# Performance work log

Hardware: AMD Instinct MI355X
Metric: run time of the kernel (lower is better)

## Reference

```python
import jax, jax.numpy as jnp
import numpy as np

H = 2048   # hidden_size
L = 512    # latent_dim
B, S = 4, 2048

def setup_inputs() -> dict:
    key = jax.random.key(0)
    ks = jax.random.split(key, 13)
    def lin(k, fan_in, shape):
        bound = 1.0 / np.sqrt(fan_in)
        return jax.random.uniform(k, shape, jnp.float32, -bound, bound)
    return {
        "hidden_states": jax.random.normal(ks[0], (B, S, H), jnp.float32),
        "num_reasoning_steps": 8,
        # to_latent: Linear(H, 2L) -> ReLU -> Linear(2L, L)
        "W_enc1": lin(ks[1], H, (2 * L, H)), "b_enc1": lin(ks[2], H, (2 * L,)),
        "W_enc2": lin(ks[3], 2 * L, (L, 2 * L)), "b_enc2": lin(ks[4], 2 * L, (L,)),
        # from_latent: Linear(L, 2L) -> ReLU -> Linear(2L, H)
        "W_dec1": lin(ks[5], L, (2 * L, L)), "b_dec1": lin(ks[6], L, (2 * L,)),
        "W_dec2": lin(ks[7], 2 * L, (H, 2 * L)), "b_dec2": lin(ks[8], 2 * L, (H,)),
        # GRUCell(L, L): weight_ih/hh [3L, L], bias_ih/hh [3L]
        "w_ih": lin(ks[9], L, (3 * L, L)), "w_hh": lin(ks[10], L, (3 * L, L)),
        "b_ih": lin(ks[11], L, (3 * L,)), "b_hh": lin(ks[12], L, (3 * L,)),
    }

def _gru_cell(x, h, w_ih, w_hh, b_ih, b_hh):
    # PyTorch GRUCell semantics
    gi = x @ w_ih.T + b_ih   # [*, 3L]
    gh = h @ w_hh.T + b_hh
    i_r, i_z, i_n = jnp.split(gi, 3, axis=-1)
    h_r, h_z, h_n = jnp.split(gh, 3, axis=-1)
    r = jax.nn.sigmoid(i_r + h_r)
    z = jax.nn.sigmoid(i_z + h_z)
    n = jnp.tanh(i_n + r * h_n)
    return (1.0 - z) * n + z * h

def reference(hidden_states, num_reasoning_steps, W_enc1, b_enc1, W_enc2, b_enc2,
              W_dec1, b_dec1, W_dec2, b_dec2, w_ih, w_hh, b_ih, b_hh):
    # encode to latent
    latent = jax.nn.relu(hidden_states @ W_enc1.T + b_enc1) @ W_enc2.T + b_enc2  # [B,S,L]

    def step(lat, _):
        lat = _gru_cell(lat, lat, w_ih, w_hh, b_ih, b_hh)
        return lat, lat

    latent, traj = jax.lax.scan(step, latent, None, length=num_reasoning_steps)
    # traj: [steps, B, S, L] -> [B, S, steps, L]
    latent_trajectory = jnp.transpose(traj, (1, 2, 0, 3))
    decoded = jax.nn.relu(latent @ W_dec1.T + b_dec1) @ W_dec2.T + b_dec2  # [B,S,H]
    return decoded, latent_trajectory
```

## Files before the change

### kernel.cpp

```cpp
#include <hip/hip_runtime.h>
#include <hip/hip_bf16.h>
#include <cstdint>
#include <cstddef>

#define TOKENS   8192
#define HID      2048
#define LAT      512
#define LAT2     1024
#define GCOLS    2048
#define STEPS    8
#define DEC_ELEMS (TOKENS*HID)

typedef __attribute__((ext_vector_type(8))) __bf16 bf16x8;
typedef __attribute__((ext_vector_type(4))) float  f32x4;

__device__ __forceinline__ unsigned short f32_to_bf16_rne(float f) {
  unsigned int u = __float_as_uint(f);
  unsigned int r = (u + 0x7FFFu + ((u >> 16) & 1u)) >> 16;
  return (unsigned short)r;
}

__device__ __forceinline__ float sigmoidf_(float x) {
  if (x >= 0.f) { float e = __expf(-x); return 1.f / (1.f + e); }
  float e = __expf(x); return e / (1.f + e);
}
__device__ __forceinline__ float tanhf_(float x) {
  float ax = fabsf(x);
  float e  = __expf(-2.f * ax);
  float t  = (1.f - e) / (1.f + e);
  return copysignf(t, x);
}

__device__ __forceinline__ void gl_lds16(const void* g, void* l) {
  __builtin_amdgcn_global_load_lds(
      (const __attribute__((address_space(1))) void*)g,
      (__attribute__((address_space(3))) void*)l, 16, 0, 0);
}

__global__ void k_cast(const float* __restrict__ s, unsigned short* __restrict__ d, int n4) {
  int i = blockIdx.x * blockDim.x + threadIdx.x;
  int stride = gridDim.x * blockDim.x;
  for (; i < n4; i += stride) {
    float4 v = ((const float4*)s)[i];
    ushort4 o;
    o.x = f32_to_bf16_rne(v.x);
    o.y = f32_to_bf16_rne(v.y);
    o.z = f32_to_bf16_rne(v.z);
    o.w = f32_to_bf16_rne(v.w);
    ((ushort4*)d)[i] = o;
  }
}

__global__ void k_gru_pack(const float* __restrict__ wih, const float* __restrict__ whh,
                           const float* __restrict__ bih, const float* __restrict__ bhh,
                           unsigned short* __restrict__ Wg, float* __restrict__ biasg) {
  int gc = blockIdx.x;
  int l  = gc >> 2;
  int g  = gc & 3;
  int row = (g == 0) ? l : (g == 1) ? (512 + l) : (1024 + l);
  for (int c = threadIdx.x; c < LAT; c += blockDim.x) {
    float v;
    if (g <= 1)      v = wih[row * LAT + c] + whh[row * LAT + c];
    else if (g == 2) v = wih[row * LAT + c];
    else             v = whh[row * LAT + c];
    Wg[(size_t)gc * LAT + c] = f32_to_bf16_rne(v);
  }
  if (threadIdx.x == 0) {
    float b;
    if (g <= 1)      b = bih[row] + bhh[row];
    else if (g == 2) b = bih[row];
    else             b = bhh[row];
    biasg[gc] = b;
  }
}

#define MWG 128
#define NWG 128
#define KTILE 64

template <int EPI>
__global__ __launch_bounds__(256)
void gemm_bt(const unsigned short* __restrict__ A,
             const unsigned short* __restrict__ W,
             const float* __restrict__ bias,
             int K, int N,
             float* __restrict__ outF,
             unsigned short* __restrict__ outB,
             const float* __restrict__ hIn,
             float* __restrict__ traj,
             int step) {
  __shared__ __align__(16) char smem[2 * MWG * KTILE * 2];
  unsigned short* As = (unsigned short*)smem;
  unsigned short* Bs = As + MWG * KTILE;

  const int tid  = threadIdx.x;
  const int lane = tid & 63;
  const int wv   = tid >> 6;
  const int wr   = wv >> 1;
  const int wc   = wv & 1;
  const int m0   = blockIdx.x * MWG;
  const int n0   = blockIdx.y * NWG;

  const int lr = lane & 15;
  const int lq = lane >> 4;

  const int srow = lane >> 3;
  const int scol = (lane & 7) * 8;

  f32x4 acc[4][4];
#pragma unroll
  for (int i = 0; i < 4; ++i)
#pragma unroll
    for (int j = 0; j < 4; ++j) acc[i][j] = (f32x4){0.f, 0.f, 0.f, 0.f};

  const unsigned short* Ab = A + (size_t)m0 * K;
  const unsigned short* Wb = W + (size_t)n0 * K;

  const int KT = K / KTILE;
  for (int kt = 0; kt < KT; ++kt) {
    const int k0 = kt * KTILE;
#pragma unroll
    for (int q = 0; q < 4; ++q) {
      int row = 32 * wv + 8 * q + srow;
      gl_lds16(Ab + (size_t)row * K + k0 + scol, As + (32 * wv + 8 * q) * KTILE);
      gl_lds16(Wb + (size_t)row * K + k0 + scol, Bs + (32 * wv + 8 * q) * KTILE);
    }
    __syncthreads();
#pragma unroll
    for (int kk = 0; kk < KTILE; kk += 32) {
      bf16x8 af[4], bf[4];
#pragma unroll
      for (int i = 0; i < 4; ++i)
        af[i] = *(const bf16x8*)(As + (wr * 64 + i * 16 + lr) * KTILE + kk + lq * 8);
#pragma unroll
      for (int j = 0; j < 4; ++j)
        bf[j] = *(const bf16x8*)(Bs + (wc * 64 + j * 16 + lr) * KTILE + kk + lq * 8);
#pragma unroll
      for (int i = 0; i < 4; ++i)
#pragma unroll
        for (int j = 0; j < 4; ++j)
          acc[i][j] = __builtin_amdgcn_mfma_f32_16x16x32_bf16(af[i], bf[j], acc[i][j], 0, 0, 0);
    }
    __syncthreads();
  }

  float bj[4];
#pragma unroll
  for (int j = 0; j < 4; ++j) bj[j] = bias[n0 + wc * 64 + j * 16 + lr];
#pragma unroll
  for (int i = 0; i < 4; ++i) {
#pragma unroll
    for (int ii = 0; ii < 4; ++ii) {
      int row = m0 + wr * 64 + i * 16 + 4 * lq + ii;
#pragma unroll
      for (int j = 0; j < 4; ++j) {
        int col = n0 + wc * 64 + j * 16 + lr;
        float v = acc[i][j][ii] + bj[j];
        if constexpr (EPI == 0) {
          v = fmaxf(v, 0.f);
          outB[(size_t)row * N + col] = f32_to_bf16_rne(v);
        } else if constexpr (EPI == 1) {
          outF[(size_t)row * N + col] = v;
          outB[(size_t)row * N + col] = f32_to_bf16_rne(v);
        } else {
          outF[(size_t)row * N + col] = v;
        }
      }
    }
  }
}


#define WAIT_LGKM0() asm volatile("s_waitcnt lgkmcnt(0)" ::: "memory")
#define WAIT_VM(n)   asm volatile("s_waitcnt vmcnt(" #n ")" ::: "memory")

#define LOAD_A(buf, mh) { \
  const int baseA = (buf)*65536 + wm*16384; \
  _Pragma("unroll") for (int m4 = 0; m4 < 4; ++m4) \
  _Pragma("unroll") for (int kki = 0; kki < 2; ++kki) { \
    int rl = (mh)*64 + m4*16 + lr; \
    int off = (rl*128 + kki*64 + lq*16) ^ ((rl & 7) << 4); \
    aR[mh][m4][kki] = *(const bf16x8*)(lds_ + baseA + off); } }

#define LOAD_B(buf, nh) { \
  const int baseB = (buf)*65536 + 32768 + (wn >> 1)*16384; \
  _Pragma("unroll") for (int n2 = 0; n2 < 2; ++n2) \
  _Pragma("unroll") for (int kki = 0; kki < 2; ++kki) { \
    int rl = (wn & 1)*64 + ((nh)*2 + n2)*16 + lr; \
    int off = (rl*128 + kki*64 + lq*16) ^ ((rl & 7) << 4); \
    bR[nh][n2][kki] = *(const bf16x8*)(lds_ + baseB + off); } }

#define STAGE_A(buf, half, kt) { \
  const unsigned short* gp = A + (size_t)(m0 + (half)*128 + rr8)*K + (size_t)(kt)*64 + cc8; \
  char* dp = lds_ + (buf)*65536 + (half)*16384 + (wv << 10); \
  gl_lds16(gp, dp); \
  gl_lds16(gp + (size_t)64*K, dp + 8192); }

#define STAGE_B(buf, half, kt) { \
  const unsigned short* gp = W + (size_t)(n0 + (half)*128 + rr8)*K + (size_t)(kt)*64 + cc8; \
  char* dp = lds_ + (buf)*65536 + 32768 + (half)*16384 + (wv << 10); \
  gl_lds16(gp, dp); \
  gl_lds16(gp + (size_t)64*K, dp + 8192); }

#define MFMAQ(mh, nh) \
  _Pragma("unroll") for (int kki = 0; kki < 2; ++kki) \
  _Pragma("unroll") for (int n2 = 0; n2 < 2; ++n2) \
  _Pragma("unroll") for (int m4 = 0; m4 < 4; ++m4) \
    acc[(mh)*4 + m4][(nh)*2 + n2] = __builtin_amdgcn_mfma_f32_16x16x32_bf16( \
        aR[mh][m4][kki], bR[nh][n2][kki], acc[(mh)*4 + m4][(nh)*2 + n2], 0, 0, 0);

#define PH_CORE(mh, nh) \
  __builtin_amdgcn_s_barrier(); \
  WAIT_LGKM0(); \
  __builtin_amdgcn_sched_barrier(0); \
  __builtin_amdgcn_s_setprio(1); \
  MFMAQ(mh, nh); \
  __builtin_amdgcn_sched_barrier(0); \
  __builtin_amdgcn_s_setprio(0);

#define PH_BAR() __builtin_amdgcn_s_barrier();

template <int EPI>
__global__ __launch_bounds__(512, 2)
void gemm256(const unsigned short* __restrict__ A,
             const unsigned short* __restrict__ W,
             const float* __restrict__ bias,
             int K, int N, int Ntiles,
             float* __restrict__ outF,
             unsigned short* __restrict__ outB,
             const float* __restrict__ hIn,
             float* __restrict__ traj,
             int step) {
  __shared__ __align__(16) char lds_[131072];

  const int tid  = threadIdx.x;
  const int lane = tid & 63;
  const int wv   = tid >> 6;
  const int wm   = wv >> 2;
  const int wn   = wv & 3;
  const int lr   = lane & 15;
  const int lq   = lane >> 4;

  const int rr8 = (wv << 3) + (lane >> 3);
  const int cc8 = ((lane & 7) ^ (lane >> 3)) << 3;

  {
  }
  const int nwg = gridDim.x;
  const int wg  = blockIdx.x;
  const int swz = (wg & 7) * (nwg >> 3) + (wg >> 3);
  const int tm  = swz / Ntiles;
  const int tn  = swz % Ntiles;
  const int m0  = tm * 256;
  const int n0  = tn * 256;

  f32x4 acc[8][4];
#pragma unroll
  for (int i = 0; i < 8; ++i)
#pragma unroll
    for (int j = 0; j < 4; ++j) acc[i][j] = (f32x4){0.f, 0.f, 0.f, 0.f};

  bf16x8 aR[2][4][2];
  bf16x8 bR[2][2][2];

  const int nIt = K >> 7;

  STAGE_B(0, 0, 0) STAGE_B(0, 1, 0) STAGE_A(0, 0, 0) STAGE_A(0, 1, 0)
  STAGE_B(1, 0, 1) STAGE_B(1, 1, 1)
  WAIT_VM(4);
  __builtin_amdgcn_s_barrier();

  for (int t = 0; t < nIt - 1; ++t) {
    const int kt1 = 2 * t + 1;
    const int kt2 = 2 * t + 2;
    const int kt3 = 2 * t + 3;
    LOAD_A(0, 0) LOAD_B(0, 0)
    STAGE_A(1, 0, kt1)
    PH_CORE(0, 0) PH_BAR()
    LOAD_B(0, 1)
    STAGE_A(1, 1, kt1)
    PH_CORE(0, 1) PH_BAR()
    LOAD_A(0, 1)
    STAGE_B(0, 0, kt2)
    PH_CORE(1, 1) PH_BAR()
    STAGE_B(0, 1, kt2)
    PH_CORE(1, 0)
    WAIT_VM(4);
    PH_BAR()
    LOAD_A(1, 0) LOAD_B(1, 0)
    STAGE_A(0, 0, kt2)
    PH_CORE(0, 0) PH_BAR()
    LOAD_B(1, 1)
    STAGE_A(0, 1, kt2)
    PH_CORE(0, 1) PH_BAR()
    LOAD_A(1, 1)
    STAGE_B(1, 0, kt3)
    PH_CORE(1, 1) PH_BAR()
    STAGE_B(1, 1, kt3)
    PH_CORE(1, 0)
    WAIT_VM(4);
    PH_BAR()
  }

  {
    const int ktL = 2 * nIt - 1;
    LOAD_A(0, 0) LOAD_B(0, 0)
    STAGE_A(1, 0, ktL)
    PH_CORE(0, 0) PH_BAR()
    LOAD_B(0, 1)
    STAGE_A(1, 1, ktL)
    PH_CORE(0, 1) PH_BAR()
    LOAD_A(0, 1)
    PH_CORE(1, 1) PH_BAR()
    PH_CORE(1, 0)
    WAIT_VM(0);
    PH_BAR()
    LOAD_A(1, 0) LOAD_B(1, 0)
    PH_CORE(0, 0) PH_BAR()
    LOAD_B(1, 1)
    PH_CORE(0, 1) PH_BAR()
    LOAD_A(1, 1)
    PH_CORE(1, 1) PH_BAR()
    PH_CORE(1, 0)
    PH_BAR()
  }

  float bj[4];
#pragma unroll
  for (int nf = 0; nf < 4; ++nf) bj[nf] = bias[n0 + wn * 64 + nf * 16 + lr];

  if constexpr (EPI == 0 || EPI == 1 || EPI == 2) {
#pragma unroll
    for (int mf = 0; mf < 8; ++mf) {
#pragma unroll
      for (int ii = 0; ii < 4; ++ii) {
        int row = m0 + wm * 128 + mf * 16 + lq * 4 + ii;
#pragma unroll
        for (int nf = 0; nf < 4; ++nf) {
          int col = n0 + wn * 64 + nf * 16 + lr;
          float v = acc[mf][nf][ii] + bj[nf];
          if constexpr (EPI == 0) {
            v = fmaxf(v, 0.f);
            outB[(size_t)row * N + col] = f32_to_bf16_rne(v);
          } else if constexpr (EPI == 1) {
            outF[(size_t)row * N + col] = v;
            outB[(size_t)row * N + col] = f32_to_bf16_rne(v);
          } else {
            outF[(size_t)row * N + col] = v;
          }
        }
      }
    }
  } else {
    float* scr = (float*)lds_ + wv * 1088;
    const int latBase = tn * 64 + wn * 16;
    const int la = lane & 15;
    const int th = lane >> 4;
#pragma unroll
    for (int mf = 0; mf < 8; ++mf) {
      WAIT_LGKM0();
#pragma unroll
      for (int nf = 0; nf < 4; ++nf)
#pragma unroll
        for (int ii = 0; ii < 4; ++ii)
          scr[(lq * 4 + ii) * 68 + nf * 16 + lr] = acc[mf][nf][ii] + bj[nf];
      WAIT_LGKM0();
#pragma unroll
      for (int tb = 0; tb < 4; ++tb) {
        int tt = th * 4 + tb;
        int token = m0 + wm * 128 + mf * 16 + tt;
        f32x4 g = *(const f32x4*)(scr + tt * 68 + la * 4);
        int latc = latBase + la;
        float h  = hIn[(size_t)token * LAT + latc];
        float r  = sigmoidf_(g.x);
        float z  = sigmoidf_(g.y);
        float n  = tanhf_(g.z + r * g.w);
        float hn = (1.f - z) * n + z * h;
        outF[(size_t)token * LAT + latc] = hn;
        outB[(size_t)token * LAT + latc] = f32_to_bf16_rne(hn);
        traj[(size_t)token * (STEPS * LAT) + step * LAT + latc] = hn;
      }
    }
  }
}

extern "C" void kernel_launch(void* const* d_in, const int* in_sizes, int n_in,
                              void* d_out, int out_size, void* d_ws, size_t ws_size,
                              hipStream_t stream) {
  const float* hs  = (const float*)d_in[0];
  const float* We1 = (const float*)d_in[2];
  const float* be1 = (const float*)d_in[3];
  const float* We2 = (const float*)d_in[4];
  const float* be2 = (const float*)d_in[5];
  const float* Wd1 = (const float*)d_in[6];
  const float* bd1 = (const float*)d_in[7];
  const float* Wd2 = (const float*)d_in[8];
  const float* bd2 = (const float*)d_in[9];
  const float* wih = (const float*)d_in[10];
  const float* whh = (const float*)d_in[11];
  const float* bih = (const float*)d_in[12];
  const float* bhh = (const float*)d_in[13];

  char* ws = (char*)d_ws;
  unsigned short* A0    = (unsigned short*)(ws + 0);
  unsigned short* We1b  = (unsigned short*)(ws + 33554432);
  unsigned short* We2b  = (unsigned short*)(ws + 37748736);
  unsigned short* Wd1b  = (unsigned short*)(ws + 38797312);
  unsigned short* Wd2b  = (unsigned short*)(ws + 39845888);
  unsigned short* Wg    = (unsigned short*)(ws + 44040192);
  float*          biasg = (float*)         (ws + 46137344);
  unsigned short* X1    = (unsigned short*)(ws + 46145536);
  float*          Lf0   = (float*)         (ws + 62922752);
  float*          Lf1   = (float*)         (ws + 79699968);
  unsigned short* Lb0   = (unsigned short*)(ws + 96477184);
  unsigned short* Lb1   = (unsigned short*)(ws + 104865792);
  unsigned short* X2    = A0;

  float* dec  = (float*)d_out;
  float* traj = (float*)d_out + DEC_ELEMS;

  k_cast<<<2048, 256, 0, stream>>>(hs,  A0,   TOKENS * HID / 4);
  k_cast<<<512,  256, 0, stream>>>(We1, We1b, LAT2 * HID / 4);
  k_cast<<<256,  256, 0, stream>>>(We2, We2b, LAT * LAT2 / 4);
  k_cast<<<256,  256, 0, stream>>>(Wd1, Wd1b, LAT2 * LAT / 4);
  k_cast<<<512,  256, 0, stream>>>(Wd2, Wd2b, HID * LAT2 / 4);
  k_gru_pack<<<GCOLS, 128, 0, stream>>>(wih, whh, bih, bhh, Wg, biasg);

  gemm256<0><<<128, 512, 0, stream>>>(A0, We1b, be1, HID, LAT2, 4,
                                      nullptr, X1, nullptr, nullptr, 0);
  gemm_bt<1><<<dim3(TOKENS / MWG, LAT / NWG), dim3(256), 0, stream>>>(
      X1, We2b, be2, LAT2, LAT, Lf0, Lb0, nullptr, nullptr, 0);
  for (int s = 0; s < STEPS; ++s) {
    const unsigned short* lbi = (s & 1) ? Lb1 : Lb0;
    const float*          lfi = (s & 1) ? Lf1 : Lf0;
    unsigned short*       lbo = (s & 1) ? Lb0 : Lb1;
    float*                lfo = (s & 1) ? Lf0 : Lf1;
    gemm256<3><<<256, 512, 0, stream>>>(lbi, Wg, biasg, LAT, GCOLS, 8,
                                        lfo, lbo, lfi, traj, s);
  }
  gemm_bt<0><<<dim3(TOKENS / MWG, LAT2 / NWG), dim3(256), 0, stream>>>(
      Lb0, Wd1b, bd1, LAT, LAT2, nullptr, X2, nullptr, nullptr, 0);
  gemm256<2><<<256, 512, 0, stream>>>(X2, Wd2b, bd2, LAT2, HID, 8,
                                      dec, nullptr, nullptr, nullptr, 0);
}
```

Baseline: 463.3 us.

## Drop fp32 latent buffers, read GRU hidden state from bf16 copy

The GRU step kernels now read the previous hidden state from the bf16 latent buffer and no longer write an fp32 copy, so the per-step fp32 read/write traffic for the latent state goes away. The encoder's second GEMM also stops writing its fp32 output. The first encoder GEMM moves from the 256-tile kernel to the 128-tile gemm_bt kernel with a larger grid. The cost is extra rounding, since the z*h term in each step now uses a bf16-rounded h and the accuracy margin gets smaller.

```diff
diff --git a/kernel.cpp b/kernel.cpp
--- a/kernel.cpp
+++ b/kernel.cpp
@@ -18,6 +18,9 @@
   unsigned int u = __float_as_uint(f);
   unsigned int r = (u + 0x7FFFu + ((u >> 16) & 1u)) >> 16;
   return (unsigned short)r;
+}
+__device__ __forceinline__ float bf16_to_f32(unsigned short u) {
+  return __uint_as_float(((unsigned int)u) << 16);
 }
 
 __device__ __forceinline__ float sigmoidf_(float x) {
@@ -85,10 +88,7 @@
              const float* __restrict__ bias,
              int K, int N,
              float* __restrict__ outF,
-             unsigned short* __restrict__ outB,
-             const float* __restrict__ hIn,
-             float* __restrict__ traj,
-             int step) {
+             unsigned short* __restrict__ outB) {
   __shared__ __align__(16) char smem[2 * MWG * KTILE * 2];
   unsigned short* As = (unsigned short*)smem;
   unsigned short* Bs = As + MWG * KTILE;
@@ -157,10 +157,8 @@
         int col = n0 + wc * 64 + j * 16 + lr;
         float v = acc[i][j][ii] + bj[j];
         if constexpr (EPI == 0) {
-          v = fmaxf(v, 0.f);
-          outB[(size_t)row * N + col] = f32_to_bf16_rne(v);
+          outB[(size_t)row * N + col] = f32_to_bf16_rne(fmaxf(v, 0.f));
         } else if constexpr (EPI == 1) {
-          outF[(size_t)row * N + col] = v;
           outB[(size_t)row * N + col] = f32_to_bf16_rne(v);
         } else {
           outF[(size_t)row * N + col] = v;
@@ -228,7 +226,7 @@
              int K, int N, int Ntiles,
              float* __restrict__ outF,
              unsigned short* __restrict__ outB,
-             const float* __restrict__ hIn,
+             const unsigned short* __restrict__ hInB,
              float* __restrict__ traj,
              int step) {
   __shared__ __align__(16) char lds_[131072];
@@ -244,8 +242,6 @@
   const int rr8 = (wv << 3) + (lane >> 3);
   const int cc8 = ((lane & 7) ^ (lane >> 3)) << 3;
 
-  {
-  }
   const int nwg = gridDim.x;
   const int wg  = blockIdx.x;
   const int swz = (wg & 7) * (nwg >> 3) + (wg >> 3);
@@ -329,7 +325,7 @@
 #pragma unroll
   for (int nf = 0; nf < 4; ++nf) bj[nf] = bias[n0 + wn * 64 + nf * 16 + lr];
 
-  if constexpr (EPI == 0 || EPI == 1 || EPI == 2) {
+  if constexpr (EPI == 2) {
 #pragma unroll
     for (int mf = 0; mf < 8; ++mf) {
 #pragma unroll
@@ -338,16 +334,7 @@
 #pragma unroll
         for (int nf = 0; nf < 4; ++nf) {
           int col = n0 + wn * 64 + nf * 16 + lr;
-          float v = acc[mf][nf][ii] + bj[nf];
-          if constexpr (EPI == 0) {
-            v = fmaxf(v, 0.f);
-            outB[(size_t)row * N + col] = f32_to_bf16_rne(v);
-          } else if constexpr (EPI == 1) {
-            outF[(size_t)row * N + col] = v;
-            outB[(size_t)row * N + col] = f32_to_bf16_rne(v);
-          } else {
-            outF[(size_t)row * N + col] = v;
-          }
+          outF[(size_t)row * N + col] = acc[mf][nf][ii] + bj[nf];
         }
       }
     }
@@ -371,12 +358,11 @@
         int token = m0 + wm * 128 + mf * 16 + tt;
         f32x4 g = *(const f32x4*)(scr + tt * 68 + la * 4);
         int latc = latBase + la;
-        float h  = hIn[(size_t)token * LAT + latc];
+        float h  = bf16_to_f32(hInB[(size_t)token * LAT + latc]);
         float r  = sigmoidf_(g.x);
         float z  = sigmoidf_(g.y);
         float n  = tanhf_(g.z + r * g.w);
         float hn = (1.f - z) * n + z * h;
-        outF[(size_t)token * LAT + latc] = hn;
         outB[(size_t)token * LAT + latc] = f32_to_bf16_rne(hn);
         traj[(size_t)token * (STEPS * LAT) + step * LAT + latc] = hn;
       }
@@ -410,10 +396,8 @@
   unsigned short* Wg    = (unsigned short*)(ws + 44040192);
   float*          biasg = (float*)         (ws + 46137344);
   unsigned short* X1    = (unsigned short*)(ws + 46145536);
-  float*          Lf0   = (float*)         (ws + 62922752);
-  float*          Lf1   = (float*)         (ws + 79699968);
-  unsigned short* Lb0   = (unsigned short*)(ws + 96477184);
-  unsigned short* Lb1   = (unsigned short*)(ws + 104865792);
+  unsigned short* Lb0   = (unsigned short*)(ws + 62922752);
+  unsigned short* Lb1   = (unsigned short*)(ws + 71311360);
   unsigned short* X2    = A0;
 
   float* dec  = (float*)d_out;
@@ -426,20 +410,18 @@
   k_cast<<<512,  256, 0, stream>>>(Wd2, Wd2b, HID * LAT2 / 4);
   k_gru_pack<<<GCOLS, 128, 0, stream>>>(wih, whh, bih, bhh, Wg, biasg);
 
-  gemm256<0><<<128, 512, 0, stream>>>(A0, We1b, be1, HID, LAT2, 4,
-                                      nullptr, X1, nullptr, nullptr, 0);
+  gemm_bt<0><<<dim3(TOKENS / MWG, LAT2 / NWG), dim3(256), 0, stream>>>(
+      A0, We1b, be1, HID, LAT2, nullptr, X1);
   gemm_bt<1><<<dim3(TOKENS / MWG, LAT / NWG), dim3(256), 0, stream>>>(
-      X1, We2b, be2, LAT2, LAT, Lf0, Lb0, nullptr, nullptr, 0);
+      X1, We2b, be2, LAT2, LAT, nullptr, Lb0);
   for (int s = 0; s < STEPS; ++s) {
     const unsigned short* lbi = (s & 1) ? Lb1 : Lb0;
-    const float*          lfi = (s & 1) ? Lf1 : Lf0;
     unsigned short*       lbo = (s & 1) ? Lb0 : Lb1;
-    float*                lfo = (s & 1) ? Lf0 : Lf1;
     gemm256<3><<<256, 512, 0, stream>>>(lbi, Wg, biasg, LAT, GCOLS, 8,
-                                        lfo, lbo, lfi, traj, s);
+                                        nullptr, lbo, lbi, traj, s);
   }
   gemm_bt<0><<<dim3(TOKENS / MWG, LAT2 / NWG), dim3(256), 0, stream>>>(
-      Lb0, Wd1b, bd1, LAT, LAT2, nullptr, X2, nullptr, nullptr, 0);
+      Lb0, Wd1b, bd1, LAT, LAT2, nullptr, X2);
   gemm256<2><<<256, 512, 0, stream>>>(X2, Wd2b, bd2, LAT2, HID, 8,
                                       dec, nullptr, nullptr, nullptr, 0);
 }
```

New measurement: 440.0 us. -5.0%, faster.
